# Kernel tuning notes

Hardware: AMD Instinct MI355X
Metric: run time of the kernel (lower is better)

The kernel has to match this reference:

```python
import jax, jax.numpy as jnp
import numpy as np

T = 0.09   # softmax temperature
M = 0.7    # momentum for key-encoder update
DIM, K, B, L, P = 128, 65536, 1024, 512, 8388608

def _l2norm(x, axis):
    return x / jnp.linalg.norm(x, axis=axis, keepdims=True)

def setup_inputs() -> dict:
    key = jax.random.key(0)
    ks = jax.random.split(key, 6)
    q = jax.random.normal(ks[0], (B, DIM), jnp.float32)
    queue = _l2norm(jax.random.normal(ks[1], (DIM, K), jnp.float32), axis=0)  # columns normalized as in __init__
    keys = jax.random.normal(ks[2], (B, DIM), jnp.float32)
    param_q = jax.random.normal(ks[3], (P,), jnp.float32)
    param_k = jax.random.normal(ks[4], (P,), jnp.float32)
    sample_idx = jax.random.randint(ks[5], (B, L), 0, K, jnp.int32)  # col 0 = positive sample index
    return {"q": q, "queue": queue, "keys": keys, "param_q": param_q,
            "param_k": param_k, "sample_idx": sample_idx, "ptr": 0}

def reference(q, queue, keys, param_q, param_k, sample_idx, ptr):
    # q = F.normalize(q, dim=1)
    qn = _l2norm(q, axis=1)
    # per-sample ragged gather of queue columns, batched: queue[:, idx] for each sample list
    cols = jnp.take(queue.T, sample_idx, axis=0)            # [B, L, DIM]
    # logits = einsum('c,ck->k', q_i, gathered_i), stacked + padded, / T
    logits = jnp.einsum('bld,bd->bl', cols, qn) / T         # [B, L]
    labels = jnp.zeros((B,), jnp.int32)                     # positive is index 0
    # momentum update of key-encoder params: k = m*k + (1-m)*q
    new_param_k = param_k * M + param_q * (1.0 - M)
    # dequeue/enqueue: queue[:, ptr:ptr+B] = normalize(keys).T (circular write)
    new_queue = jax.lax.dynamic_update_slice(queue, _l2norm(keys, axis=1).T, (0, ptr))
    return (logits, labels, new_queue, new_param_k)
```

## Files before the change

### kernel.cpp

```cpp
#include <hip/hip_runtime.h>
#include <stdint.h>

#define DIM   128
#define KCOLS 65536
#define BB    1024
#define LL    512
#define PSZ   8388608
#define INV_T (1.0f / 0.09f)
#define MOM   0.7f

#define OUT_LOGITS 0
#define OUT_LABELS (BB * LL)
#define OUT_QUEUE  (BB * LL + BB)
#define OUT_PARAMK (BB * LL + BB + DIM * KCOLS)

#define WS_QT 0
#define WS_QN (KCOLS * DIM * 2)
#define WS_KN (WS_QN + BB * DIM * 4)

__device__ inline unsigned short f32_to_bf16(float f) {
    uint32_t u = __float_as_uint(f);
    uint32_t r = (u + 0x7fffu + ((u >> 16) & 1u)) >> 16;
    return (unsigned short)r;
}

__global__ void norm_kernel(const float* __restrict__ q,
                            const float* __restrict__ keys,
                            float* __restrict__ qn, float* __restrict__ kn) {
    int w    = threadIdx.x >> 6;
    int lane = threadIdx.x & 63;
    int row  = blockIdx.x * 4 + w;
    const float* src;
    float* dst;
    int r;
    if (row < BB) { src = q;    dst = qn; r = row; }
    else          { src = keys; dst = kn; r = row - BB; }
    float2 v = *(const float2*)&src[r * DIM + lane * 2];
    float s  = v.x * v.x + v.y * v.y;
#pragma unroll
    for (int m = 32; m >= 1; m >>= 1) s += __shfl_xor(s, m, 64);
    float inv = 1.0f / sqrtf(s);
    float2 o  = {v.x * inv, v.y * inv};
    *(float2*)&dst[r * DIM + lane * 2] = o;
}

__global__ void param_kernel(const float* __restrict__ pq,
                             const float* __restrict__ pk,
                             float* __restrict__ out) {
    int gid  = blockIdx.x * blockDim.x + threadIdx.x;
    float4 a = ((const float4*)pq)[gid];
    float4 b = ((const float4*)pk)[gid];
    float4 r;
    r.x = b.x * MOM + a.x * (1.0f - MOM);
    r.y = b.y * MOM + a.y * (1.0f - MOM);
    r.z = b.z * MOM + a.z * (1.0f - MOM);
    r.w = b.w * MOM + a.w * (1.0f - MOM);
    ((float4*)(out + OUT_PARAMK))[gid] = r;
    if (gid < BB) out[OUT_LABELS + gid] = 0.0f;
}

__global__ void queue_fused_kernel(const float* __restrict__ queue,
                                   const float* __restrict__ kn,
                                   const int* __restrict__ ptr_p,
                                   float* __restrict__ outq,
                                   unsigned short* __restrict__ qt) {
    __shared__ float tile[64][DIM + 1];
    int k0 = blockIdx.x * 64;
    int t  = threadIdx.x;
    int ptr   = ptr_p[0];
    int start = min(max(ptr, 0), KCOLS - BB);

    int lane16 = t & 15;
    int hi     = t >> 4;
    int kq     = lane16 * 4;
#pragma unroll
    for (int p = 0; p < 8; ++p) {
        int d = p * 16 + hi;
        float4 v = *(const float4*)&queue[(size_t)d * KCOLS + k0 + kq];
        float vv[4] = {v.x, v.y, v.z, v.w};
#pragma unroll
        for (int j = 0; j < 4; ++j) {
            tile[kq + j][d] = vv[j];
            int col = k0 + kq + j;
            if (col >= start && col < start + BB)
                vv[j] = kn[(size_t)(col - start) * DIM + d];
        }
        float4 w = {vv[0], vv[1], vv[2], vv[3]};
        *(float4*)&outq[(size_t)d * KCOLS + k0 + kq] = w;
    }
    __syncthreads();
    int d0 = lane16 * 8;
#pragma unroll
    for (int ki = 0; ki < 4; ++ki) {
        int kl = hi + ki * 16;
        float f[8];
#pragma unroll
        for (int j = 0; j < 8; ++j) f[j] = tile[kl][d0 + j];
        uint4 o;
        o.x = (uint32_t)f32_to_bf16(f[0]) | ((uint32_t)f32_to_bf16(f[1]) << 16);
        o.y = (uint32_t)f32_to_bf16(f[2]) | ((uint32_t)f32_to_bf16(f[3]) << 16);
        o.z = (uint32_t)f32_to_bf16(f[4]) | ((uint32_t)f32_to_bf16(f[5]) << 16);
        o.w = (uint32_t)f32_to_bf16(f[6]) | ((uint32_t)f32_to_bf16(f[7]) << 16);
        *(uint4*)&qt[(size_t)(k0 + kl) * DIM + d0] = o;
    }
}

__global__ void __launch_bounds__(256)
logits_kernel(const float* __restrict__ qn,
              const unsigned short* __restrict__ qt,
              const int* __restrict__ sidx,
              float* __restrict__ out_logits) {
    int b   = blockIdx.x >> 3;
    int xcd = blockIdx.x & 7;
    int t   = threadIdx.x;

    __shared__ unsigned short lst[LL];
    __shared__ int n;
    if (t == 0) n = 0;
    __syncthreads();
#pragma unroll
    for (int l = t; l < LL; l += 256) {
        int idx = sidx[b * LL + l];
        if ((idx >> 13) == xcd) {
            int p = atomicAdd(&n, 1);
            lst[p] = (unsigned short)l;
        }
    }
    __syncthreads();
    int cnt = n;

    int quarter = t & 3;
    int grp     = t >> 2;

    float qreg[32];
    const float4* qb = (const float4*)(qn + b * DIM + quarter * 32);
#pragma unroll
    for (int i = 0; i < 8; ++i) {
        float4 v = qb[i];
        qreg[4 * i + 0] = v.x; qreg[4 * i + 1] = v.y;
        qreg[4 * i + 2] = v.z; qreg[4 * i + 3] = v.w;
    }

    for (int i = grp; i < cnt; i += 64) {
        int l   = lst[i];
        int idx = sidx[b * LL + l];
        const uint4* p = (const uint4*)(qt + (size_t)idx * DIM + quarter * 32);
        float s0 = 0.f, s1 = 0.f, s2 = 0.f, s3 = 0.f;
#pragma unroll
        for (int c = 0; c < 4; ++c) {
            uint4 u = p[c];
            float acc = 0.f;
            acc += qreg[c * 8 + 0] * __uint_as_float(u.x << 16);
            acc += qreg[c * 8 + 1] * __uint_as_float(u.x & 0xffff0000u);
            acc += qreg[c * 8 + 2] * __uint_as_float(u.y << 16);
            acc += qreg[c * 8 + 3] * __uint_as_float(u.y & 0xffff0000u);
            acc += qreg[c * 8 + 4] * __uint_as_float(u.z << 16);
            acc += qreg[c * 8 + 5] * __uint_as_float(u.z & 0xffff0000u);
            acc += qreg[c * 8 + 6] * __uint_as_float(u.w << 16);
            acc += qreg[c * 8 + 7] * __uint_as_float(u.w & 0xffff0000u);
            if (c == 0) s0 = acc; else if (c == 1) s1 = acc;
            else if (c == 2) s2 = acc; else s3 = acc;
        }
        float s = (s0 + s1) + (s2 + s3);
        s += __shfl_xor(s, 1, 64);
        s += __shfl_xor(s, 2, 64);
        if (quarter == 0) out_logits[b * LL + l] = s * INV_T;
    }
}

extern "C" void kernel_launch(void* const* d_in, const int* in_sizes, int n_in,
                              void* d_out, int out_size, void* d_ws, size_t ws_size,
                              hipStream_t stream) {
    const float* q     = (const float*)d_in[0];
    const float* queue = (const float*)d_in[1];
    const float* keys  = (const float*)d_in[2];
    const float* pq    = (const float*)d_in[3];
    const float* pk    = (const float*)d_in[4];
    const int*   sidx  = (const int*)d_in[5];
    const int*   ptr_p = (const int*)d_in[6];
    float* out = (float*)d_out;

    unsigned short* ws_qt = (unsigned short*)((char*)d_ws + WS_QT);
    float* ws_qn = (float*)((char*)d_ws + WS_QN);
    float* ws_kn = (float*)((char*)d_ws + WS_KN);

    norm_kernel<<<512, 256, 0, stream>>>(q, keys, ws_qn, ws_kn);
    queue_fused_kernel<<<KCOLS / 64, 256, 0, stream>>>(queue, ws_kn, ptr_p,
                                                       out + OUT_QUEUE, ws_qt);
    param_kernel<<<PSZ / 4 / 256, 256, 0, stream>>>(pq, pk, out);
    logits_kernel<<<BB * 8, 256, 0, stream>>>(ws_qn, ws_qt, sidx,
                                              out + OUT_LOGITS);
}
```

Baseline: 214.5 us.

## Fuse normalization into queue and logits kernels, merge param update, prefetch gathers

Removes the separate norm kernel. Key normalization now happens inside the queue transpose kernel and query normalization (with 1/T folded in) inside the logits kernel. The momentum parameter update is merged into the logits launch as extra blocks, cutting the launch count from four to two. The logits kernel drops the per-XCD index partitioning, so each block handles a whole row and software-pipelines its bf16 gather loads four deep. This trades L2 locality of the XCD split for fewer launches and more memory-level parallelism.

New measurement: 188.0 us. -12.3%, faster.

```diff
diff --git a/kernel.cpp b/kernel.cpp
--- a/kernel.cpp
+++ b/kernel.cpp
@@ -15,8 +15,6 @@
 #define OUT_PARAMK (BB * LL + BB + DIM * KCOLS)
 
 #define WS_QT 0
-#define WS_QN (KCOLS * DIM * 2)
-#define WS_KN (WS_QN + BB * DIM * 4)
 
 __device__ inline unsigned short f32_to_bf16(float f) {
     uint32_t u = __float_as_uint(f);
@@ -24,52 +22,39 @@
     return (unsigned short)r;
 }
 
-__global__ void norm_kernel(const float* __restrict__ q,
-                            const float* __restrict__ keys,
-                            float* __restrict__ qn, float* __restrict__ kn) {
-    int w    = threadIdx.x >> 6;
-    int lane = threadIdx.x & 63;
-    int row  = blockIdx.x * 4 + w;
-    const float* src;
-    float* dst;
-    int r;
-    if (row < BB) { src = q;    dst = qn; r = row; }
-    else          { src = keys; dst = kn; r = row - BB; }
-    float2 v = *(const float2*)&src[r * DIM + lane * 2];
-    float s  = v.x * v.x + v.y * v.y;
-#pragma unroll
-    for (int m = 32; m >= 1; m >>= 1) s += __shfl_xor(s, m, 64);
-    float inv = 1.0f / sqrtf(s);
-    float2 o  = {v.x * inv, v.y * inv};
-    *(float2*)&dst[r * DIM + lane * 2] = o;
-}
-
-__global__ void param_kernel(const float* __restrict__ pq,
-                             const float* __restrict__ pk,
-                             float* __restrict__ out) {
-    int gid  = blockIdx.x * blockDim.x + threadIdx.x;
-    float4 a = ((const float4*)pq)[gid];
-    float4 b = ((const float4*)pk)[gid];
-    float4 r;
-    r.x = b.x * MOM + a.x * (1.0f - MOM);
-    r.y = b.y * MOM + a.y * (1.0f - MOM);
-    r.z = b.z * MOM + a.z * (1.0f - MOM);
-    r.w = b.w * MOM + a.w * (1.0f - MOM);
-    ((float4*)(out + OUT_PARAMK))[gid] = r;
-    if (gid < BB) out[OUT_LABELS + gid] = 0.0f;
-}
-
-__global__ void queue_fused_kernel(const float* __restrict__ queue,
-                                   const float* __restrict__ kn,
-                                   const int* __restrict__ ptr_p,
-                                   float* __restrict__ outq,
-                                   unsigned short* __restrict__ qt) {
+__global__ void __launch_bounds__(256)
+queue_fused_kernel(const float* __restrict__ queue,
+                   const float* __restrict__ keys,
+                   const int* __restrict__ ptr_p,
+                   float* __restrict__ outq,
+                   unsigned short* __restrict__ qt) {
     __shared__ float tile[64][DIM + 1];
+    __shared__ float invn_s[64];
     int k0 = blockIdx.x * 64;
     int t  = threadIdx.x;
     int ptr   = ptr_p[0];
     int start = min(max(ptr, 0), KCOLS - BB);
 
+    {
+        int row_local = t >> 2;
+        int l4        = t & 3;
+        int c = k0 + row_local;
+        if (c >= start && c < start + BB) {
+            const float4* kr =
+                (const float4*)&keys[(size_t)(c - start) * DIM + l4 * 32];
+            float s = 0.f;
+#pragma unroll
+            for (int i = 0; i < 8; ++i) {
+                float4 v = kr[i];
+                s += v.x * v.x + v.y * v.y + v.z * v.z + v.w * v.w;
+            }
+            s += __shfl_xor(s, 1, 64);
+            s += __shfl_xor(s, 2, 64);
+            if (l4 == 0) invn_s[row_local] = 1.0f / sqrtf(s);
+        }
+    }
+    __syncthreads();
+
     int lane16 = t & 15;
     int hi     = t >> 4;
     int kq     = lane16 * 4;
@@ -83,7 +68,7 @@
             tile[kq + j][d] = vv[j];
             int col = k0 + kq + j;
             if (col >= start && col < start + BB)
-                vv[j] = kn[(size_t)(col - start) * DIM + d];
+                vv[j] = keys[(size_t)(col - start) * DIM + d] * invn_s[kq + j];
         }
         float4 w = {vv[0], vv[1], vv[2], vv[3]};
         *(float4*)&outq[(size_t)d * KCOLS + k0 + kq] = w;
@@ -105,66 +90,98 @@
     }
 }
 
+#define DOT8(uu, qo, dst) {                                    \
+    float acc = 0.f;                                           \
+    acc += qreg[(qo) + 0] * __uint_as_float((uu).x << 16);     \
+    acc += qreg[(qo) + 1] * __uint_as_float((uu).x & 0xffff0000u); \
+    acc += qreg[(qo) + 2] * __uint_as_float((uu).y << 16);     \
+    acc += qreg[(qo) + 3] * __uint_as_float((uu).y & 0xffff0000u); \
+    acc += qreg[(qo) + 4] * __uint_as_float((uu).z << 16);     \
+    acc += qreg[(qo) + 5] * __uint_as_float((uu).z & 0xffff0000u); \
+    acc += qreg[(qo) + 6] * __uint_as_float((uu).w << 16);     \
+    acc += qreg[(qo) + 7] * __uint_as_float((uu).w & 0xffff0000u); \
+    (dst) = acc; }
+
 __global__ void __launch_bounds__(256)
-logits_kernel(const float* __restrict__ qn,
-              const unsigned short* __restrict__ qt,
-              const int* __restrict__ sidx,
-              float* __restrict__ out_logits) {
-    int b   = blockIdx.x >> 3;
-    int xcd = blockIdx.x & 7;
-    int t   = threadIdx.x;
-
-    __shared__ unsigned short lst[LL];
-    __shared__ int n;
-    if (t == 0) n = 0;
-    __syncthreads();
-#pragma unroll
-    for (int l = t; l < LL; l += 256) {
-        int idx = sidx[b * LL + l];
-        if ((idx >> 13) == xcd) {
-            int p = atomicAdd(&n, 1);
-            lst[p] = (unsigned short)l;
-        }
-    }
-    __syncthreads();
-    int cnt = n;
+logits_param_kernel(const float* __restrict__ q,
+                    const unsigned short* __restrict__ qt,
+                    const int* __restrict__ sidx,
+                    const float* __restrict__ pq,
+                    const float* __restrict__ pk,
+                    float* __restrict__ out) {
+    int t = threadIdx.x;
+
+    if (blockIdx.x >= BB) {
+        int gid  = (blockIdx.x - BB) * 256 + t;
+        float4 a = ((const float4*)pq)[gid];
+        float4 c = ((const float4*)pk)[gid];
+        float4 r;
+        r.x = c.x * MOM + a.x * (1.0f - MOM);
+        r.y = c.y * MOM + a.y * (1.0f - MOM);
+        r.z = c.z * MOM + a.z * (1.0f - MOM);
+        r.w = c.w * MOM + a.w * (1.0f - MOM);
+        ((float4*)(out + OUT_PARAMK))[gid] = r;
+        if (gid < BB) out[OUT_LABELS + gid] = 0.0f;
+        return;
+    }
+
+    int b = blockIdx.x;
+    __shared__ int sl[LL];
+#pragma unroll
+    for (int l = t; l < LL; l += 256) sl[l] = sidx[b * LL + l];
 
     int quarter = t & 3;
     int grp     = t >> 2;
 
     float qreg[32];
-    const float4* qb = (const float4*)(qn + b * DIM + quarter * 32);
-#pragma unroll
-    for (int i = 0; i < 8; ++i) {
-        float4 v = qb[i];
-        qreg[4 * i + 0] = v.x; qreg[4 * i + 1] = v.y;
-        qreg[4 * i + 2] = v.z; qreg[4 * i + 3] = v.w;
-    }
-
-    for (int i = grp; i < cnt; i += 64) {
-        int l   = lst[i];
-        int idx = sidx[b * LL + l];
-        const uint4* p = (const uint4*)(qt + (size_t)idx * DIM + quarter * 32);
-        float s0 = 0.f, s1 = 0.f, s2 = 0.f, s3 = 0.f;
-#pragma unroll
-        for (int c = 0; c < 4; ++c) {
-            uint4 u = p[c];
-            float acc = 0.f;
-            acc += qreg[c * 8 + 0] * __uint_as_float(u.x << 16);
-            acc += qreg[c * 8 + 1] * __uint_as_float(u.x & 0xffff0000u);
-            acc += qreg[c * 8 + 2] * __uint_as_float(u.y << 16);
-            acc += qreg[c * 8 + 3] * __uint_as_float(u.y & 0xffff0000u);
-            acc += qreg[c * 8 + 4] * __uint_as_float(u.z << 16);
-            acc += qreg[c * 8 + 5] * __uint_as_float(u.z & 0xffff0000u);
-            acc += qreg[c * 8 + 6] * __uint_as_float(u.w << 16);
-            acc += qreg[c * 8 + 7] * __uint_as_float(u.w & 0xffff0000u);
-            if (c == 0) s0 = acc; else if (c == 1) s1 = acc;
-            else if (c == 2) s2 = acc; else s3 = acc;
-        }
+    {
+        const float4* qb = (const float4*)(q + (size_t)b * DIM + quarter * 32);
+        float s = 0.f;
+#pragma unroll
+        for (int i = 0; i < 8; ++i) {
+            float4 v = qb[i];
+            qreg[4 * i + 0] = v.x; qreg[4 * i + 1] = v.y;
+            qreg[4 * i + 2] = v.z; qreg[4 * i + 3] = v.w;
+            s += v.x * v.x + v.y * v.y + v.z * v.z + v.w * v.w;
+        }
+        s += __shfl_xor(s, 1, 64);
+        s += __shfl_xor(s, 2, 64);
+        float inv = rsqrtf(s) * INV_T;
+#pragma unroll
+        for (int i = 0; i < 32; ++i) qreg[i] *= inv;
+    }
+    __syncthreads();
+
+    int idxs[8];
+#pragma unroll
+    for (int e = 0; e < 8; ++e) idxs[e] = sl[grp + (e << 6)];
+
+    uint4 u[4][4];
+#pragma unroll
+    for (int e = 0; e < 4; ++e) {
+        const uint4* p = (const uint4*)(qt + (size_t)idxs[e] * DIM) + quarter * 4;
+        u[e][0] = p[0]; u[e][1] = p[1]; u[e][2] = p[2]; u[e][3] = p[3];
+    }
+#pragma unroll
+    for (int e = 0; e < 8; ++e) {
+        const int slot = e & 3;
+        uint4 t0 = u[slot][0], t1 = u[slot][1], t2 = u[slot][2], t3 = u[slot][3];
+        if (e < 4) {
+            const uint4* p =
+                (const uint4*)(qt + (size_t)idxs[e + 4] * DIM) + quarter * 4;
+            u[slot][0] = p[0]; u[slot][1] = p[1];
+            u[slot][2] = p[2]; u[slot][3] = p[3];
+        }
+        float s0, s1, s2, s3;
+        DOT8(t0,  0, s0);
+        DOT8(t1,  8, s1);
+        DOT8(t2, 16, s2);
+        DOT8(t3, 24, s3);
         float s = (s0 + s1) + (s2 + s3);
         s += __shfl_xor(s, 1, 64);
         s += __shfl_xor(s, 2, 64);
-        if (quarter == 0) out_logits[b * LL + l] = s * INV_T;
+        if (quarter == 0)
+            out[OUT_LOGITS + (size_t)b * LL + grp + (e << 6)] = s;
     }
 }
 
@@ -181,13 +198,9 @@
     float* out = (float*)d_out;
 
     unsigned short* ws_qt = (unsigned short*)((char*)d_ws + WS_QT);
-    float* ws_qn = (float*)((char*)d_ws + WS_QN);
-    float* ws_kn = (float*)((char*)d_ws + WS_KN);
-
-    norm_kernel<<<512, 256, 0, stream>>>(q, keys, ws_qn, ws_kn);
-    queue_fused_kernel<<<KCOLS / 64, 256, 0, stream>>>(queue, ws_kn, ptr_p,
+
+    queue_fused_kernel<<<KCOLS / 64, 256, 0, stream>>>(queue, keys, ptr_p,
                                                        out + OUT_QUEUE, ws_qt);
-    param_kernel<<<PSZ / 4 / 256, 256, 0, stream>>>(pq, pk, out);
-    logits_kernel<<<BB * 8, 256, 0, stream>>>(ws_qn, ws_qt, sidx,
-                                              out + OUT_LOGITS);
-}
+    logits_param_kernel<<<BB + PSZ / 1024, 256, 0, stream>>>(q, ws_qt, sidx,
+                                                             pq, pk, out);
+}
```
